# Kernel tuning notes

Hardware: AMD Instinct MI355X
Metric: run time of the kernel (lower is better)

Reference implementation:

```python
import jax, jax.numpy as jnp
import numpy as np

B, C, H, W = 16, 256, 96, 96
P = 16          # num_prototypes
G = 8           # GroupNorm groups
EPS = 1e-5


def setup_inputs() -> dict:
    key = jax.random.key(0)
    ks = jax.random.split(key, 18)
    n = jax.random.normal
    return {
        "x": n(ks[0], (B, C, H, W), jnp.float32),
        "prototypes": n(ks[1], (1, P, C), jnp.float32),
        "pos_embed": n(ks[2], (1, C, 64, 64), jnp.float32) * 0.02,
        "q_w": n(ks[3], (C, C), jnp.float32) * (C ** -0.5),
        "q_b": n(ks[4], (C,), jnp.float32) * 0.01,
        "k_w": n(ks[5], (C, C), jnp.float32) * (C ** -0.5),
        "k_b": n(ks[6], (C,), jnp.float32) * 0.01,
        "v_w": n(ks[7], (C, C), jnp.float32) * (C ** -0.5),
        "v_b": n(ks[8], (C,), jnp.float32) * 0.01,
        "out_w": n(ks[9], (C, C), jnp.float32) * (C ** -0.5),
        "out_b": n(ks[10], (C,), jnp.float32) * 0.01,
        "dw_w": n(ks[11], (C, 1, 3, 3), jnp.float32) * (1.0 / 3.0),  # depthwise 3x3, no bias
        "bn_g": 1.0 + 0.1 * n(ks[12], (C,), jnp.float32),
        "bn_b": 0.1 * n(ks[13], (C,), jnp.float32),
        "bn_mean": 0.05 * n(ks[14], (C,), jnp.float32),
        "bn_var": 0.5 + jax.random.uniform(ks[15], (C,), jnp.float32),
        "gn_g": 1.0 + 0.1 * n(ks[16], (C,), jnp.float32),
        "gn_b": 0.1 * n(ks[17], (C,), jnp.float32),
    }


def _forward(x, prototypes, pos_embed, q_w, q_b, k_w, k_b, v_w, v_b,
             out_w, out_b, dw_w, bn_g, bn_b, bn_mean, bn_var, gn_g, gn_b):
    b, c, h, w = x.shape
    residual = x

    # bilinear interpolation of learnable PE (half-pixel centers == align_corners=False)
    pos = jax.image.resize(pos_embed, (1, c, h, w), method="bilinear")
    xp = x + pos

    # 1x1 conv Q projection -> [B, HW, C]
    q = jnp.einsum("bchw,dc->bhwd", xp, q_w) + q_b          # [B,H,W,C]
    q = q.reshape(b, h * w, c)

    # K/V from tiny prototype set (shared across batch) -> [P, C]
    k = prototypes[0] @ k_w.T + k_b
    v = prototypes[0] @ v_w.T + v_b

    # attention over only P=16 keys
    scale = c ** (-0.5)
    attn = jax.nn.softmax(jnp.einsum("bnc,pc->bnp", q, k) * scale, axis=-1)
    out = jnp.einsum("bnp,pc->bnc", attn, v)                # [B,HW,C]
    out = out.reshape(b, h, w, c).transpose(0, 3, 1, 2)     # [B,C,H,W]

    # 1x1 conv out projection
    out = jnp.einsum("bchw,dc->bdhw", out, out_w) + out_b[None, :, None, None]

    # local branch: depthwise 3x3 conv -> BN (eval, running stats) -> GELU(exact)
    dw = jax.lax.conv_general_dilated(
        out, dw_w, window_strides=(1, 1), padding="SAME",
        feature_group_count=c, dimension_numbers=("NCHW", "OIHW", "NCHW"))
    inv = (bn_g / jnp.sqrt(bn_var + EPS))[None, :, None, None]
    bn = (dw - bn_mean[None, :, None, None]) * inv + bn_b[None, :, None, None]
    out = out + jax.nn.gelu(bn, approximate=False)

    # GroupNorm(8, C) over residual sum
    y = out + residual
    yg = y.reshape(b, G, c // G, h, w)
    mu = yg.mean(axis=(2, 3, 4), keepdims=True)
    var = yg.var(axis=(2, 3, 4), keepdims=True)
    yn = ((yg - mu) * jax.lax.rsqrt(var + EPS)).reshape(b, c, h, w)
    return yn * gn_g[None, :, None, None] + gn_b[None, :, None, None]


def reference(x, prototypes, pos_embed, q_w, q_b, k_w, k_b, v_w, v_b,
              out_w, out_b, dw_w, bn_g, bn_b, bn_mean, bn_var, gn_g, gn_b):
    return _forward(x, prototypes, pos_embed, q_w, q_b, k_w, k_b, v_w, v_b,
                    out_w, out_b, dw_w, bn_g, bn_b, bn_mean, bn_var, gn_g, gn_b)
```

## Files before the change

kernel.cpp:

```cpp
#include <hip/hip_runtime.h>
#include <math.h>

#define C_   256
#define B_   16
#define HW_  9216
#define W_   96
#define H_   96
#define P_   16
#define EPS_ 1e-5f

typedef unsigned int u32;

__global__ __launch_bounds__(256) void k_kv(
    const float* __restrict__ proto, const float* __restrict__ kw,
    const float* __restrict__ kb, const float* __restrict__ vw,
    const float* __restrict__ vb, float* __restrict__ wk, float* __restrict__ wv)
{
    __shared__ float pr[C_];
    const int p = blockIdx.x, d = threadIdx.x;
    pr[d] = proto[p * C_ + d];
    __syncthreads();
    float kk = kb[d], vv = vb[d];
    const float* kr = kw + d * C_;
    const float* vr = vw + d * C_;
    #pragma unroll 8
    for (int c = 0; c < C_; ++c) {
        const float pc = pr[c];
        kk = fmaf(pc, kr[c], kk);
        vv = fmaf(pc, vr[c], vv);
    }
    wk[p * C_ + d] = kk;
    wv[p * C_ + d] = vv;
}

__global__ __launch_bounds__(256) void k_mu(
    const float* __restrict__ wk, const float* __restrict__ wv,
    const float* __restrict__ qw, const float* __restrict__ qb,
    const float* __restrict__ ow,
    float* __restrict__ wm, float* __restrict__ wu, float* __restrict__ ws0)
{
    __shared__ float row[C_];
    __shared__ float red[C_];
    const int blk = blockIdx.x, t = threadIdx.x;
    if (blk < 16) {
        const int p = blk;
        row[t] = wk[p * C_ + t];
        __syncthreads();
        float mm = 0.f;
        #pragma unroll 8
        for (int d = 0; d < C_; ++d)
            mm = fmaf(row[d], qw[d * C_ + t], mm);
        wm[t * P_ + p] = mm;
        red[t] = qb[t] * row[t];
        __syncthreads();
        for (int s = 128; s > 0; s >>= 1) {
            if (t < s) red[t] += red[t + s];
            __syncthreads();
        }
        if (t == 0) ws0[p] = red[0];
    } else {
        const int p = blk - 16;
        row[t] = wv[p * C_ + t];
        __syncthreads();
        float uu = 0.f;
        const float* orow = ow + t * C_;
        #pragma unroll 8
        for (int c = 0; c < C_; ++c)
            uu = fmaf(row[c], orow[c], uu);
        wu[t * P_ + p] = uu;
    }
}

__global__ __launch_bounds__(256) void k_pd(
    const float* __restrict__ pos, const float* __restrict__ m,
    float* __restrict__ pd)
{
    const int n = blockIdx.x * 256 + threadIdx.x;
    const int h = n / W_, w = n - h * W_;
    float sy = (h + 0.5f) * (2.0f / 3.0f) - 0.5f;
    float sx = (w + 0.5f) * (2.0f / 3.0f) - 0.5f;
    sy = fminf(fmaxf(sy, 0.f), 63.f);
    sx = fminf(fmaxf(sx, 0.f), 63.f);
    const int y0 = (int)sy, x0 = (int)sx;
    const float fy = sy - (float)y0, fx = sx - (float)x0;
    const int y1 = min(y0 + 1, 63), x1 = min(x0 + 1, 63);
    const float w00 = (1.f - fy) * (1.f - fx), w01 = (1.f - fy) * fx;
    const float w10 = fy * (1.f - fx),         w11 = fy * fx;
    const int i00 = y0 * 64 + x0, i01 = y0 * 64 + x1;
    const int i10 = y1 * 64 + x0, i11 = y1 * 64 + x1;

    float acc[P_];
    #pragma unroll
    for (int p = 0; p < P_; ++p) acc[p] = 0.f;

    #pragma unroll 4
    for (int c = 0; c < C_; ++c) {
        const float* pc = pos + c * 4096;
        const float pv = pc[i00] * w00 + pc[i01] * w01 +
                         pc[i10] * w10 + pc[i11] * w11;
        #pragma unroll
        for (int p = 0; p < P_; ++p)
            acc[p] = fmaf(pv, m[c * P_ + p], acc[p]);
    }
    #pragma unroll
    for (int p = 0; p < P_; ++p) pd[p * HW_ + n] = acc[p];
}

__global__ __launch_bounds__(256) void k_attn(
    const float* __restrict__ x, const float* __restrict__ m,
    const float* __restrict__ u, const float* __restrict__ s0,
    const float* __restrict__ pd, const float* __restrict__ outb,
    float* __restrict__ o2)
{
    const int b = blockIdx.y;
    const int n = blockIdx.x * 256 + threadIdx.x;
    const float* xp = x + (size_t)b * (C_ * HW_) + n;

    float acc[P_];
    #pragma unroll
    for (int p = 0; p < P_; ++p) acc[p] = 0.f;

    for (int c0 = 0; c0 < C_; c0 += 8) {
        float xv[8];
        #pragma unroll
        for (int j = 0; j < 8; ++j)
            xv[j] = xp[(size_t)(c0 + j) * HW_];
        #pragma unroll
        for (int j = 0; j < 8; ++j) {
            const float* mr = m + (c0 + j) * P_;
            #pragma unroll
            for (int p = 0; p < P_; ++p)
                acc[p] = fmaf(xv[j], mr[p], acc[p]);
        }
    }

    float l[P_];
    float mx = -1e30f;
    #pragma unroll
    for (int p = 0; p < P_; ++p) {
        l[p] = (acc[p] + pd[p * HW_ + n] + s0[p]) * 0.0625f;
        mx = fmaxf(mx, l[p]);
    }
    float sum = 0.f;
    #pragma unroll
    for (int p = 0; p < P_; ++p) { l[p] = __expf(l[p] - mx); sum += l[p]; }
    const float r = 1.f / sum;
    #pragma unroll
    for (int p = 0; p < P_; ++p) l[p] *= r;

    float* op = o2 + (size_t)b * (C_ * HW_) + n;
    #pragma unroll 4
    for (int d = 0; d < C_; ++d) {
        float o = outb[d];
        #pragma unroll
        for (int p = 0; p < P_; ++p)
            o = fmaf(l[p], u[d * P_ + p], o);
        op[(size_t)d * HW_] = o;
    }
}

__global__ __launch_bounds__(256) void k_local(
    const float* __restrict__ x,
    const float* __restrict__ dww, const float* __restrict__ bng,
    const float* __restrict__ bnb, const float* __restrict__ bnm,
    const float* __restrict__ bnv,
    float* __restrict__ y, float* __restrict__ sums)
{
    __shared__ float tile[98 * 98];
    __shared__ float red[512];
    const int c = blockIdx.x, b = blockIdx.y, t = threadIdx.x;

    if (t < 98) { tile[t] = 0.f; tile[97 * 98 + t] = 0.f; }
    if (t < 96) { tile[(t + 1) * 98] = 0.f; tile[(t + 1) * 98 + 97] = 0.f; }

    const size_t plane = (size_t)(b * C_ + c) * HW_;
    const float* op = y + plane;
    #pragma unroll 4
    for (int k = 0; k < 36; ++k) {
        const int i = t + k * 256;
        const int h = i / W_, w = i - h * W_;
        tile[(h + 1) * 98 + (w + 1)] = op[i];
    }
    __syncthreads();

    const float w00 = dww[c * 9 + 0], w01 = dww[c * 9 + 1], w02 = dww[c * 9 + 2];
    const float w10 = dww[c * 9 + 3], w11 = dww[c * 9 + 4], w12 = dww[c * 9 + 5];
    const float w20 = dww[c * 9 + 6], w21 = dww[c * 9 + 7], w22 = dww[c * 9 + 8];
    const float inv  = bng[c] * rsqrtf(bnv[c] + EPS_);
    const float mu   = bnm[c];
    const float beta = bnb[c];

    const float* xp = x + plane;
    float* yp = y + plane;
    float s1 = 0.f, s2 = 0.f;

    #pragma unroll 4
    for (int k = 0; k < 36; ++k) {
        const int i = t + k * 256;
        const float xv = xp[i];
        const int h = i / W_, w = i - h * W_;
        const float* ctr = &tile[(h + 1) * 98 + (w + 1)];
        float dwv = ctr[-99] * w00 + ctr[-98] * w01 + ctr[-97] * w02
                  + ctr[-1]  * w10 + ctr[0]   * w11 + ctr[1]   * w12
                  + ctr[97]  * w20 + ctr[98]  * w21 + ctr[99]  * w22;
        const float bn = (dwv - mu) * inv + beta;
        const float g  = 0.5f * bn * (1.f + erff(bn * 0.70710678118654752f));
        const float yv = ctr[0] + g + xv;
        s1 += yv;
        s2 = fmaf(yv, yv, s2);
        yp[i] = yv;
    }

    red[t] = s1; red[256 + t] = s2;
    __syncthreads();
    for (int s = 128; s > 0; s >>= 1) {
        if (t < s) { red[t] += red[t + s]; red[256 + t] += red[256 + t + s]; }
        __syncthreads();
    }
    if (t == 0) {
        const int bg = b * 8 + (c >> 5);
        atomicAdd(&sums[bg * 2 + 0], red[0]);
        atomicAdd(&sums[bg * 2 + 1], red[256]);
    }
}

__global__ __launch_bounds__(256) void k_norm(
    const float* __restrict__ sums, const float* __restrict__ gng,
    const float* __restrict__ gnb, float* __restrict__ y)
{
    const u32 i0 = ((u32)blockIdx.x * 256u + threadIdx.x) * 4u;
    const u32 plane = i0 / HW_;
    const u32 c = plane & 255u;
    const u32 b = plane >> 8;
    const u32 bg = b * 8u + (c >> 5);
    const float cntinv = 1.f / 294912.f;
    const float mean = sums[bg * 2 + 0] * cntinv;
    const float var  = fmaf(sums[bg * 2 + 1], cntinv, -mean * mean);
    const float inv  = rsqrtf(var + EPS_);
    const float a  = gng[c] * inv;
    const float bb = gnb[c] - mean * a;

    float4 v = *reinterpret_cast<const float4*>(y + i0);
    v.x = fmaf(v.x, a, bb);
    v.y = fmaf(v.y, a, bb);
    v.z = fmaf(v.z, a, bb);
    v.w = fmaf(v.w, a, bb);
    *reinterpret_cast<float4*>(y + i0) = v;
}

extern "C" void kernel_launch(void* const* d_in, const int* in_sizes, int n_in,
                              void* d_out, int out_size, void* d_ws, size_t ws_size,
                              hipStream_t stream)
{
    const float* x     = (const float*)d_in[0];
    const float* proto = (const float*)d_in[1];
    const float* pos   = (const float*)d_in[2];
    const float* qw    = (const float*)d_in[3];
    const float* qb    = (const float*)d_in[4];
    const float* kw    = (const float*)d_in[5];
    const float* kb    = (const float*)d_in[6];
    const float* vw    = (const float*)d_in[7];
    const float* vb    = (const float*)d_in[8];
    const float* ow    = (const float*)d_in[9];
    const float* ob    = (const float*)d_in[10];
    const float* dww   = (const float*)d_in[11];
    const float* bng   = (const float*)d_in[12];
    const float* bnb   = (const float*)d_in[13];
    const float* bnm   = (const float*)d_in[14];
    const float* bnv   = (const float*)d_in[15];
    const float* gng   = (const float*)d_in[16];
    const float* gnb   = (const float*)d_in[17];

    char* ws = (char*)d_ws;
    float* sums = (float*)(ws);
    float* s0   = (float*)(ws + 1024);
    float* wk   = (float*)(ws + 2048);
    float* wv   = (float*)(ws + 2048 + 16384);
    float* wm   = (float*)(ws + 2048 + 2 * 16384);
    float* wu   = (float*)(ws + 2048 + 3 * 16384);
    float* pd   = (float*)(ws + 2048 + 4 * 16384);

    float* out = (float*)d_out;

    hipMemsetAsync(sums, 0, 1024, stream);
    k_kv<<<16, 256, 0, stream>>>(proto, kw, kb, vw, vb, wk, wv);
    k_mu<<<32, 256, 0, stream>>>(wk, wv, qw, qb, ow, wm, wu, s0);
    k_pd<<<36, 256, 0, stream>>>(pos, wm, pd);
    k_attn<<<dim3(36, 16), 256, 0, stream>>>(x, wm, wu, s0, pd, ob, out);
    k_local<<<dim3(256, 16), 256, 0, stream>>>(x, dww, bng, bnb, bnm, bnv, out, sums);
    k_norm<<<36864, 256, 0, stream>>>(sums, gng, gnb, out);
}
```

Baseline: 563.7 us.

## Vectorize attention and depthwise kernels, fold sums memset into k_kv

k_attn now handles two pixels per thread using float2 loads and stores, so each weight read is shared across two outputs and the grid shrinks to half. k_local fills its shared tile with float4 global loads into a padded 100-wide layout and computes four outputs per thread from float4 shared reads. It also reuses the tile for the reduction buffer. The separate memset of the GroupNorm sums is replaced by zeroing inside k_kv, removing one launch. The cost is more register pressure, lower occupancy in k_attn because it has half as many blocks, and a dependency on 8- and 16-byte alignment.

```diff
diff --git a/kernel.cpp b/kernel.cpp
--- a/kernel.cpp
+++ b/kernel.cpp
@@ -14,10 +14,12 @@
 __global__ __launch_bounds__(256) void k_kv(
     const float* __restrict__ proto, const float* __restrict__ kw,
     const float* __restrict__ kb, const float* __restrict__ vw,
-    const float* __restrict__ vb, float* __restrict__ wk, float* __restrict__ wv)
+    const float* __restrict__ vb, float* __restrict__ wk, float* __restrict__ wv,
+    float* __restrict__ sums)
 {
     __shared__ float pr[C_];
     const int p = blockIdx.x, d = threadIdx.x;
+    if (p == 0) sums[d] = 0.f;
     pr[d] = proto[p * C_ + d];
     __syncthreads();
     float kk = kb[d], vv = vb[d];
@@ -113,49 +115,60 @@
     float* __restrict__ o2)
 {
     const int b = blockIdx.y;
-    const int n = blockIdx.x * 256 + threadIdx.x;
-    const float* xp = x + (size_t)b * (C_ * HW_) + n;
-
-    float acc[P_];
-    #pragma unroll
-    for (int p = 0; p < P_; ++p) acc[p] = 0.f;
-
-    for (int c0 = 0; c0 < C_; c0 += 8) {
-        float xv[8];
+    const int n0 = (blockIdx.x * 256 + threadIdx.x) * 2;
+    const float* xp = x + (size_t)b * (C_ * HW_) + n0;
+
+    float acc0[P_], acc1[P_];
+    #pragma unroll
+    for (int p = 0; p < P_; ++p) { acc0[p] = 0.f; acc1[p] = 0.f; }
+
+    for (int cc = 0; cc < C_; cc += 8) {
+        float2 xv[8];
         #pragma unroll
         for (int j = 0; j < 8; ++j)
-            xv[j] = xp[(size_t)(c0 + j) * HW_];
+            xv[j] = *reinterpret_cast<const float2*>(xp + (size_t)(cc + j) * HW_);
         #pragma unroll
         for (int j = 0; j < 8; ++j) {
-            const float* mr = m + (c0 + j) * P_;
+            const float* mr = m + (cc + j) * P_;
             #pragma unroll
-            for (int p = 0; p < P_; ++p)
-                acc[p] = fmaf(xv[j], mr[p], acc[p]);
+            for (int p = 0; p < P_; ++p) {
+                acc0[p] = fmaf(xv[j].x, mr[p], acc0[p]);
+                acc1[p] = fmaf(xv[j].y, mr[p], acc1[p]);
+            }
         }
     }
 
-    float l[P_];
-    float mx = -1e30f;
+    float l0[P_], l1[P_];
+    float mx0 = -1e30f, mx1 = -1e30f;
     #pragma unroll
     for (int p = 0; p < P_; ++p) {
-        l[p] = (acc[p] + pd[p * HW_ + n] + s0[p]) * 0.0625f;
-        mx = fmaxf(mx, l[p]);
-    }
-    float sum = 0.f;
-    #pragma unroll
-    for (int p = 0; p < P_; ++p) { l[p] = __expf(l[p] - mx); sum += l[p]; }
-    const float r = 1.f / sum;
-    #pragma unroll
-    for (int p = 0; p < P_; ++p) l[p] *= r;
-
-    float* op = o2 + (size_t)b * (C_ * HW_) + n;
+        const float2 pv = *reinterpret_cast<const float2*>(pd + (size_t)p * HW_ + n0);
+        l0[p] = (acc0[p] + pv.x + s0[p]) * 0.0625f;
+        l1[p] = (acc1[p] + pv.y + s0[p]) * 0.0625f;
+        mx0 = fmaxf(mx0, l0[p]);
+        mx1 = fmaxf(mx1, l1[p]);
+    }
+    float sum0 = 0.f, sum1 = 0.f;
+    #pragma unroll
+    for (int p = 0; p < P_; ++p) {
+        l0[p] = __expf(l0[p] - mx0); sum0 += l0[p];
+        l1[p] = __expf(l1[p] - mx1); sum1 += l1[p];
+    }
+    const float r0 = 1.f / sum0, r1 = 1.f / sum1;
+    #pragma unroll
+    for (int p = 0; p < P_; ++p) { l0[p] *= r0; l1[p] *= r1; }
+
+    float* op = o2 + (size_t)b * (C_ * HW_) + n0;
     #pragma unroll 4
     for (int d = 0; d < C_; ++d) {
-        float o = outb[d];
-        #pragma unroll
-        for (int p = 0; p < P_; ++p)
-            o = fmaf(l[p], u[d * P_ + p], o);
-        op[(size_t)d * HW_] = o;
+        const float* ur = u + d * P_;
+        float o0 = outb[d], o1 = o0;
+        #pragma unroll
+        for (int p = 0; p < P_; ++p) {
+            o0 = fmaf(l0[p], ur[p], o0);
+            o1 = fmaf(l1[p], ur[p], o1);
+        }
+        *reinterpret_cast<float2*>(op + (size_t)d * HW_) = make_float2(o0, o1);
     }
 }
 
@@ -166,20 +179,23 @@
     const float* __restrict__ bnv,
     float* __restrict__ y, float* __restrict__ sums)
 {
-    __shared__ float tile[98 * 98];
-    __shared__ float red[512];
+    __shared__ float tile[98 * 100];
     const int c = blockIdx.x, b = blockIdx.y, t = threadIdx.x;
 
-    if (t < 98) { tile[t] = 0.f; tile[97 * 98 + t] = 0.f; }
-    if (t < 96) { tile[(t + 1) * 98] = 0.f; tile[(t + 1) * 98 + 97] = 0.f; }
+    if (t < 100) { tile[t] = 0.f; tile[97 * 100 + t] = 0.f; }
+    if (t < 96)  { tile[(t + 1) * 100 + 1] = 0.f; tile[(t + 1) * 100 + 98] = 0.f; }
 
     const size_t plane = (size_t)(b * C_ + c) * HW_;
-    const float* op = y + plane;
-    #pragma unroll 4
-    for (int k = 0; k < 36; ++k) {
-        const int i = t + k * 256;
-        const int h = i / W_, w = i - h * W_;
-        tile[(h + 1) * 98 + (w + 1)] = op[i];
+    const float4* op4 = reinterpret_cast<const float4*>(y + plane);
+    #pragma unroll
+    for (int k = 0; k < 9; ++k) {
+        const int g = t + k * 256;
+        const int h = g / 24;
+        const int w0 = (g - h * 24) * 4;
+        const float4 v = op4[g];
+        const int base = (h + 1) * 100 + w0 + 2;
+        *reinterpret_cast<float2*>(&tile[base])     = make_float2(v.x, v.y);
+        *reinterpret_cast<float2*>(&tile[base + 2]) = make_float2(v.z, v.w);
     }
     __syncthreads();
 
@@ -190,27 +206,45 @@
     const float mu   = bnm[c];
     const float beta = bnb[c];
 
-    const float* xp = x + plane;
-    float* yp = y + plane;
+    const float4* xp4 = reinterpret_cast<const float4*>(x + plane);
+    float4* yp4 = reinterpret_cast<float4*>(y + plane);
     float s1 = 0.f, s2 = 0.f;
 
-    #pragma unroll 4
-    for (int k = 0; k < 36; ++k) {
-        const int i = t + k * 256;
-        const float xv = xp[i];
-        const int h = i / W_, w = i - h * W_;
-        const float* ctr = &tile[(h + 1) * 98 + (w + 1)];
-        float dwv = ctr[-99] * w00 + ctr[-98] * w01 + ctr[-97] * w02
-                  + ctr[-1]  * w10 + ctr[0]   * w11 + ctr[1]   * w12
-                  + ctr[97]  * w20 + ctr[98]  * w21 + ctr[99]  * w22;
-        const float bn = (dwv - mu) * inv + beta;
-        const float g  = 0.5f * bn * (1.f + erff(bn * 0.70710678118654752f));
-        const float yv = ctr[0] + g + xv;
-        s1 += yv;
-        s2 = fmaf(yv, yv, s2);
-        yp[i] = yv;
-    }
-
+    #pragma unroll
+    for (int k = 0; k < 9; ++k) {
+        const int g = t + k * 256;
+        const float4 xv = xp4[g];
+        const int h = g / 24;
+        const int w0 = (g - h * 24) * 4;
+        const int r0 = h * 100 + w0;
+        const float4 a0 = *reinterpret_cast<const float4*>(&tile[r0]);
+        const float4 a1 = *reinterpret_cast<const float4*>(&tile[r0 + 4]);
+        const float4 b0 = *reinterpret_cast<const float4*>(&tile[r0 + 100]);
+        const float4 b1 = *reinterpret_cast<const float4*>(&tile[r0 + 104]);
+        const float4 c0 = *reinterpret_cast<const float4*>(&tile[r0 + 200]);
+        const float4 c1 = *reinterpret_cast<const float4*>(&tile[r0 + 204]);
+        const float A[8]  = {a0.x, a0.y, a0.z, a0.w, a1.x, a1.y, a1.z, a1.w};
+        const float Bv[8] = {b0.x, b0.y, b0.z, b0.w, b1.x, b1.y, b1.z, b1.w};
+        const float Cv[8] = {c0.x, c0.y, c0.z, c0.w, c1.x, c1.y, c1.z, c1.w};
+        const float xs[4] = {xv.x, xv.y, xv.z, xv.w};
+        float ys[4];
+        #pragma unroll
+        for (int j = 0; j < 4; ++j) {
+            float dwv = A[j + 1] * w00 + A[j + 2] * w01 + A[j + 3] * w02
+                      + Bv[j + 1] * w10 + Bv[j + 2] * w11 + Bv[j + 3] * w12
+                      + Cv[j + 1] * w20 + Cv[j + 2] * w21 + Cv[j + 3] * w22;
+            const float bn = (dwv - mu) * inv + beta;
+            const float gl = 0.5f * bn * (1.f + erff(bn * 0.70710678118654752f));
+            const float yv = Bv[j + 2] + gl + xs[j];
+            s1 += yv;
+            s2 = fmaf(yv, yv, s2);
+            ys[j] = yv;
+        }
+        yp4[g] = make_float4(ys[0], ys[1], ys[2], ys[3]);
+    }
+
+    __syncthreads();
+    float* red = tile;
     red[t] = s1; red[256 + t] = s2;
     __syncthreads();
     for (int s = 128; s > 0; s >>= 1) {
@@ -282,11 +316,10 @@
 
     float* out = (float*)d_out;
 
-    hipMemsetAsync(sums, 0, 1024, stream);
-    k_kv<<<16, 256, 0, stream>>>(proto, kw, kb, vw, vb, wk, wv);
+    k_kv<<<16, 256, 0, stream>>>(proto, kw, kb, vw, vb, wk, wv, sums);
     k_mu<<<32, 256, 0, stream>>>(wk, wv, qw, qb, ow, wm, wu, s0);
     k_pd<<<36, 256, 0, stream>>>(pos, wm, pd);
-    k_attn<<<dim3(36, 16), 256, 0, stream>>>(x, wm, wu, s0, pd, ob, out);
+    k_attn<<<dim3(18, 16), 256, 0, stream>>>(x, wm, wu, s0, pd, ob, out);
     k_local<<<dim3(256, 16), 256, 0, stream>>>(x, dww, bng, bnb, bnm, bnv, out, sums);
     k_norm<<<36864, 256, 0, stream>>>(sums, gng, gnb, out);
 }
```

After: 533.4 us. 5.4% less time.
